# Kernel optimization log

Hardware: AMD Instinct MI355X
Metric: run time of the kernel (lower is better)

The kernel has to match this reference:

```python
import jax, jax.numpy as jnp
import numpy as np

N_NODES = 50000
N_EDGES = 500000
D = 128  # node/edge feature dim


def setup_inputs() -> dict:
    key = jax.random.key(0)
    k1, k2, k3, k4, k5 = jax.random.split(key, 5)
    x_node = jax.random.normal(k1, (N_NODES, D), dtype=jnp.float32)
    x_edge = jax.random.normal(k2, (N_EDGES, D), dtype=jnp.float32)
    edge_index = jax.random.randint(k3, (N_EDGES, 2), 0, N_NODES, dtype=jnp.int64)
    # MLP params: Linear(3D -> D) -> ReLU -> Linear(D -> D)
    W1 = jax.random.normal(k4, (3 * D, D), dtype=jnp.float32) * (1.0 / np.sqrt(3 * D))
    b1 = jnp.zeros((D,), dtype=jnp.float32)
    W2 = jax.random.normal(k5, (D, D), dtype=jnp.float32) * (1.0 / np.sqrt(D))
    b2 = jnp.zeros((D,), dtype=jnp.float32)
    return {"x_node": x_node, "x_edge": x_edge, "edge_index": edge_index,
            "W1": W1, "b1": b1, "W2": W2, "b2": b2}


def reference(x_node, x_edge, edge_index, W1, b1, W2, b2):
    # gather node features at both endpoints of each edge
    v0 = x_node[edge_index[:, 0]]          # [E, D]
    v1 = x_node[edge_index[:, 1]]          # [E, D]
    x_new = jnp.concatenate([v0, v1, x_edge], axis=1)  # [E, 3D]
    h = jax.nn.relu(x_new @ W1 + b1)       # [E, D]
    x_edge_new = h @ W2 + b2               # [E, D]
    return x_edge_new
```

## Files before the change

### kernel.cpp

```cpp
#include <hip/hip_runtime.h>
#include <stdint.h>

#define D 128
#define MT 64

typedef short short8 __attribute__((ext_vector_type(8)));
typedef float f32x16 __attribute__((ext_vector_type(16)));

__device__ __forceinline__ unsigned short f2bf(float f) {
    union { float f; uint32_t u; } v;
    v.f = f;
    uint32_t u = v.u;
    uint32_t r = (u + 0x7fffu + ((u >> 16) & 1u)) >> 16;
    return (unsigned short)r;
}

__global__ void pack_weights_kernel(const float* __restrict__ W1,
                                    const float* __restrict__ W2,
                                    unsigned short* __restrict__ W1p,
                                    unsigned short* __restrict__ W2p) {
    int t = blockIdx.x * 256 + threadIdx.x;
    if (t < 6144) {
        int kt = t >> 8, nt = (t >> 6) & 3, lane = t & 63;
        int n = nt * 32 + (lane & 31);
        int kb = kt * 16 + (lane >> 5) * 8;
        unsigned short* dst = W1p + t * 8;
        #pragma unroll
        for (int j = 0; j < 8; ++j) dst[j] = f2bf(W1[(kb + j) * D + n]);
    } else if (t < 8192) {
        int u = t - 6144;
        int kt = u >> 8, nt = (u >> 6) & 3, lane = u & 63;
        int n = nt * 32 + (lane & 31);
        int kb = kt * 16 + (lane >> 5) * 8;
        unsigned short* dst = W2p + u * 8;
        #pragma unroll
        for (int j = 0; j < 8; ++j) dst[j] = f2bf(W2[(kb + j) * D + n]);
    }
}

__global__ __launch_bounds__(512, 6) void edge_mlp_kernel(
    const float* __restrict__ x_node,
    const float* __restrict__ x_edge,
    const int* __restrict__ eidx,
    const unsigned short* __restrict__ W1p,
    const unsigned short* __restrict__ W2p,
    const float* __restrict__ b1,
    const float* __restrict__ b2,
    float* __restrict__ out,
    int E) {
    __shared__ unsigned short lds[MT * 392];
    unsigned short* Hs = lds;

    const int t = threadIdx.x;
    const int r0 = blockIdx.x * MT;

    const int w = t >> 6;
    const int cb = w & 3;
    const int rt = w >> 2;
    const int lane = t & 63;
    const int lrow = lane & 31;
    const int khalf = (lane >> 5) * 8;
    const int n = cb * 32 + lrow;
    const int rbump = (lane >> 5) * 4;
    const int arow = rt * 32 + lrow;

    const unsigned short* bp1 = W1p + ((size_t)cb * 64 + lane) * 8;
    const unsigned short* bp2 = W2p + ((size_t)cb * 64 + lane) * 8;

    short8 bbuf0 = *(const short8*)(bp1);
    short8 bbuf1 = *(const short8*)(bp1 + 1 * 2048);
    short8 bbuf2 = *(const short8*)(bp1 + 2 * 2048);
    short8 bbuf3 = *(const short8*)(bp1 + 3 * 2048);

    {
        const int lane32 = t & 31;
        const int rsub = t >> 5;

        int2 e[4];
        int rgc[4];
        #pragma unroll
        for (int rb = 0; rb < 4; ++rb) {
            int rg = r0 + rb * 16 + rsub;
            rgc[rb] = rg < E ? rg : E - 1;
            e[rb] = ((const int2*)eidx)[rgc[rb]];
        }
        float4 v0[4], v1[4], v2[4];
        #pragma unroll
        for (int rb = 0; rb < 4; ++rb) {
            v0[rb] = ((const float4*)(x_node + (size_t)e[rb].x * D))[lane32];
            v1[rb] = ((const float4*)(x_node + (size_t)e[rb].y * D))[lane32];
            v2[rb] = ((const float4*)(x_edge + (size_t)rgc[rb] * D))[lane32];
        }
        #pragma unroll
        for (int rb = 0; rb < 4; ++rb) {
            int row = rb * 16 + rsub;
            unsigned short* base = &lds[row * 392 + lane32 * 4];
            ushort4 p;
            p.x = f2bf(v0[rb].x); p.y = f2bf(v0[rb].y); p.z = f2bf(v0[rb].z); p.w = f2bf(v0[rb].w);
            *(ushort4*)(base) = p;
            p.x = f2bf(v1[rb].x); p.y = f2bf(v1[rb].y); p.z = f2bf(v1[rb].z); p.w = f2bf(v1[rb].w);
            *(ushort4*)(base + 128) = p;
            p.x = f2bf(v2[rb].x); p.y = f2bf(v2[rb].y); p.z = f2bf(v2[rb].z); p.w = f2bf(v2[rb].w);
            *(ushort4*)(base + 256) = p;
        }
    }
    __syncthreads();

    f32x16 acc;
    #pragma unroll
    for (int i = 0; i < 16; ++i) acc[i] = 0.f;

    #pragma unroll
    for (int kt = 0; kt < 24; ++kt) {
        short8 a = *(const short8*)&lds[arow * 392 + kt * 16 + khalf];
        short8 b;
        switch (kt & 3) {
            case 0: b = bbuf0; if (kt + 4 < 24) bbuf0 = *(const short8*)(bp1 + (kt + 4) * 2048); break;
            case 1: b = bbuf1; if (kt + 4 < 24) bbuf1 = *(const short8*)(bp1 + (kt + 4) * 2048); break;
            case 2: b = bbuf2; if (kt + 4 < 24) bbuf2 = *(const short8*)(bp1 + (kt + 4) * 2048); break;
            default: b = bbuf3; if (kt + 4 < 24) bbuf3 = *(const short8*)(bp1 + (kt + 4) * 2048); break;
        }
        acc = __builtin_amdgcn_mfma_f32_32x32x16_bf16(a, b, acc, 0, 0, 0);
    }

    short8 b2buf[8];
    #pragma unroll
    for (int i = 0; i < 8; ++i) b2buf[i] = *(const short8*)(bp2 + i * 2048);

    __syncthreads();

    {
        float b1v = b1[n];
        #pragma unroll
        for (int r = 0; r < 16; ++r) {
            int rr = rt * 32 + (r & 3) + 8 * (r >> 2) + rbump;
            Hs[rr * 136 + n] = f2bf(fmaxf(acc[r] + b1v, 0.f));
        }
    }
    __syncthreads();

    f32x16 c;
    #pragma unroll
    for (int i = 0; i < 16; ++i) c[i] = 0.f;

    #pragma unroll
    for (int kt = 0; kt < 8; ++kt) {
        short8 a = *(const short8*)&Hs[arow * 136 + kt * 16 + khalf];
        c = __builtin_amdgcn_mfma_f32_32x32x16_bf16(a, b2buf[kt], c, 0, 0, 0);
    }

    {
        float b2v = b2[n];
        #pragma unroll
        for (int r = 0; r < 16; ++r) {
            int rr = rt * 32 + (r & 3) + 8 * (r >> 2) + rbump;
            int rg = r0 + rr;
            if (rg < E) out[(size_t)rg * D + n] = c[r] + b2v;
        }
    }
}

extern "C" void kernel_launch(void* const* d_in, const int* in_sizes, int n_in,
                              void* d_out, int out_size, void* d_ws, size_t ws_size,
                              hipStream_t stream) {
    const float* x_node = (const float*)d_in[0];
    const float* x_edge = (const float*)d_in[1];
    const int*   eidx   = (const int*)d_in[2];
    const float* W1     = (const float*)d_in[3];
    const float* b1     = (const float*)d_in[4];
    const float* W2     = (const float*)d_in[5];
    const float* b2     = (const float*)d_in[6];
    float* out = (float*)d_out;

    const int E = in_sizes[1] / D;

    unsigned short* W1p = (unsigned short*)d_ws;
    unsigned short* W2p = W1p + 6144 * 8;

    pack_weights_kernel<<<32, 256, 0, stream>>>(W1, W2, W1p, W2p);

    int nblk = (E + MT - 1) / MT;
    edge_mlp_kernel<<<nblk, 512, 0, stream>>>(x_node, x_edge, eidx, W1p, W2p, b1, b2, out, E);
}
```

Before: 533.4 us.

## Make edge MLP kernel persistent with register-prefetched gathers for upcoming tiles

Launches a fixed grid of at most 512 blocks that loop over 64-edge tiles. Each iteration gathers the node and edge features for the next tile into registers, and the edge indices for the tile after that, while the current tile's two MFMA GEMMs run. X and H get separate LDS buffers so staging and compute do not alias. This aims to hide the latency of the random gathers behind compute. In exchange it lowers the launch-bound occupancy hint and reloads weight fragments from global memory on every tile instead of keeping them in a register ring.

```diff
diff --git a/kernel.cpp b/kernel.cpp
--- a/kernel.cpp
+++ b/kernel.cpp
@@ -3,6 +3,8 @@
 
 #define D 128
 #define MT 64
+#define XS 392
+#define HS 136
 
 typedef short short8 __attribute__((ext_vector_type(8)));
 typedef float f32x16 __attribute__((ext_vector_type(16)));
@@ -38,7 +40,7 @@
     }
 }
 
-__global__ __launch_bounds__(512, 6) void edge_mlp_kernel(
+__global__ __launch_bounds__(512, 4) void edge_mlp_kernel(
     const float* __restrict__ x_node,
     const float* __restrict__ x_edge,
     const int* __restrict__ eidx,
@@ -47,13 +49,16 @@
     const float* __restrict__ b1,
     const float* __restrict__ b2,
     float* __restrict__ out,
-    int E) {
-    __shared__ unsigned short lds[MT * 392];
-    unsigned short* Hs = lds;
+    int E, int nblk) {
+    __shared__ unsigned short Xs[MT * XS];
+    __shared__ unsigned short Hs[MT * HS];
 
     const int t = threadIdx.x;
-    const int r0 = blockIdx.x * MT;
+    const int g = gridDim.x;
+    const int bid = blockIdx.x;
 
+    const int lane32 = t & 31;
+    const int rsub = t >> 5;
     const int w = t >> 6;
     const int cb = w & 3;
     const int rt = w >> 2;
@@ -66,96 +71,104 @@
 
     const unsigned short* bp1 = W1p + ((size_t)cb * 64 + lane) * 8;
     const unsigned short* bp2 = W2p + ((size_t)cb * 64 + lane) * 8;
+    const float b1v = b1[n];
+    const float b2v = b2[n];
 
-    short8 bbuf0 = *(const short8*)(bp1);
-    short8 bbuf1 = *(const short8*)(bp1 + 1 * 2048);
-    short8 bbuf2 = *(const short8*)(bp1 + 2 * 2048);
-    short8 bbuf3 = *(const short8*)(bp1 + 3 * 2048);
+    int2 e[4];
+    int rg[4];
+    float4 v0[4], v1[4], v2[4];
 
     {
-        const int lane32 = t & 31;
-        const int rsub = t >> 5;
-
-        int2 e[4];
-        int rgc[4];
+        int tb = bid * MT;
         #pragma unroll
         for (int rb = 0; rb < 4; ++rb) {
-            int rg = r0 + rb * 16 + rsub;
-            rgc[rb] = rg < E ? rg : E - 1;
-            e[rb] = ((const int2*)eidx)[rgc[rb]];
+            int r = tb + rb * 16 + rsub;
+            rg[rb] = r < E ? r : E - 1;
+            e[rb] = ((const int2*)eidx)[rg[rb]];
         }
-        float4 v0[4], v1[4], v2[4];
         #pragma unroll
         for (int rb = 0; rb < 4; ++rb) {
             v0[rb] = ((const float4*)(x_node + (size_t)e[rb].x * D))[lane32];
             v1[rb] = ((const float4*)(x_node + (size_t)e[rb].y * D))[lane32];
-            v2[rb] = ((const float4*)(x_edge + (size_t)rgc[rb] * D))[lane32];
+            v2[rb] = ((const float4*)(x_edge + (size_t)rg[rb] * D))[lane32];
         }
+        int nt2 = bid + g < nblk ? bid + g : nblk - 1;
+        int tb2 = nt2 * MT;
         #pragma unroll
         for (int rb = 0; rb < 4; ++rb) {
-            int row = rb * 16 + rsub;
-            unsigned short* base = &lds[row * 392 + lane32 * 4];
+            int r = tb2 + rb * 16 + rsub;
+            rg[rb] = r < E ? r : E - 1;
+            e[rb] = ((const int2*)eidx)[rg[rb]];
+        }
+    }
+
+    for (int tile = bid; tile < nblk; tile += g) {
+        #pragma unroll
+        for (int rb = 0; rb < 4; ++rb) {
+            unsigned short* base = &Xs[(rb * 16 + rsub) * XS + lane32 * 4];
             ushort4 p;
-            p.x = f2bf(v0[rb].x); p.y = f2bf(v0[rb].y); p.z = f2bf(v0[rb].z); p.w = f2bf(v0[rb].w);
+            p.x = f2bf(v0[rb].x); p.y = f2bf(v0[rb].y);
+            p.z = f2bf(v0[rb].z); p.w = f2bf(v0[rb].w);
             *(ushort4*)(base) = p;
-            p.x = f2bf(v1[rb].x); p.y = f2bf(v1[rb].y); p.z = f2bf(v1[rb].z); p.w = f2bf(v1[rb].w);
+            p.x = f2bf(v1[rb].x); p.y = f2bf(v1[rb].y);
+            p.z = f2bf(v1[rb].z); p.w = f2bf(v1[rb].w);
             *(ushort4*)(base + 128) = p;
-            p.x = f2bf(v2[rb].x); p.y = f2bf(v2[rb].y); p.z = f2bf(v2[rb].z); p.w = f2bf(v2[rb].w);
+            p.x = f2bf(v2[rb].x); p.y = f2bf(v2[rb].y);
+            p.z = f2bf(v2[rb].z); p.w = f2bf(v2[rb].w);
             *(ushort4*)(base + 256) = p;
         }
-    }
-    __syncthreads();
+        __syncthreads();
 
-    f32x16 acc;
-    #pragma unroll
-    for (int i = 0; i < 16; ++i) acc[i] = 0.f;
+        #pragma unroll
+        for (int rb = 0; rb < 4; ++rb) {
+            v0[rb] = ((const float4*)(x_node + (size_t)e[rb].x * D))[lane32];
+            v1[rb] = ((const float4*)(x_node + (size_t)e[rb].y * D))[lane32];
+            v2[rb] = ((const float4*)(x_edge + (size_t)rg[rb] * D))[lane32];
+        }
+        {
+            int nt2 = tile + 2 * g < nblk ? tile + 2 * g : nblk - 1;
+            int tb2 = nt2 * MT;
+            #pragma unroll
+            for (int rb = 0; rb < 4; ++rb) {
+                int r = tb2 + rb * 16 + rsub;
+                rg[rb] = r < E ? r : E - 1;
+                e[rb] = ((const int2*)eidx)[rg[rb]];
+            }
+        }
 
-    #pragma unroll
-    for (int kt = 0; kt < 24; ++kt) {
-        short8 a = *(const short8*)&lds[arow * 392 + kt * 16 + khalf];
-        short8 b;
-        switch (kt & 3) {
-            case 0: b = bbuf0; if (kt + 4 < 24) bbuf0 = *(const short8*)(bp1 + (kt + 4) * 2048); break;
-            case 1: b = bbuf1; if (kt + 4 < 24) bbuf1 = *(const short8*)(bp1 + (kt + 4) * 2048); break;
-            case 2: b = bbuf2; if (kt + 4 < 24) bbuf2 = *(const short8*)(bp1 + (kt + 4) * 2048); break;
-            default: b = bbuf3; if (kt + 4 < 24) bbuf3 = *(const short8*)(bp1 + (kt + 4) * 2048); break;
+        f32x16 acc;
+        #pragma unroll
+        for (int i = 0; i < 16; ++i) acc[i] = 0.f;
+        #pragma unroll 8
+        for (int kt = 0; kt < 24; ++kt) {
+            short8 a = *(const short8*)&Xs[arow * XS + kt * 16 + khalf];
+            short8 b = *(const short8*)(bp1 + (size_t)kt * 2048);
+            acc = __builtin_amdgcn_mfma_f32_32x32x16_bf16(a, b, acc, 0, 0, 0);
         }
-        acc = __builtin_amdgcn_mfma_f32_32x32x16_bf16(a, b, acc, 0, 0, 0);
-    }
-
-    short8 b2buf[8];
-    #pragma unroll
-    for (int i = 0; i < 8; ++i) b2buf[i] = *(const short8*)(bp2 + i * 2048);
-
-    __syncthreads();
-
-    {
-        float b1v = b1[n];
         #pragma unroll
         for (int r = 0; r < 16; ++r) {
             int rr = rt * 32 + (r & 3) + 8 * (r >> 2) + rbump;
-            Hs[rr * 136 + n] = f2bf(fmaxf(acc[r] + b1v, 0.f));
+            Hs[rr * HS + n] = f2bf(fmaxf(acc[r] + b1v, 0.f));
         }
-    }
-    __syncthreads();
+        __syncthreads();
 
-    f32x16 c;
-    #pragma unroll
-    for (int i = 0; i < 16; ++i) c[i] = 0.f;
-
-    #pragma unroll
-    for (int kt = 0; kt < 8; ++kt) {
-        short8 a = *(const short8*)&Hs[arow * 136 + kt * 16 + khalf];
-        c = __builtin_amdgcn_mfma_f32_32x32x16_bf16(a, b2buf[kt], c, 0, 0, 0);
-    }
-
-    {
-        float b2v = b2[n];
+        f32x16 c;
         #pragma unroll
-        for (int r = 0; r < 16; ++r) {
-            int rr = rt * 32 + (r & 3) + 8 * (r >> 2) + rbump;
-            int rg = r0 + rr;
-            if (rg < E) out[(size_t)rg * D + n] = c[r] + b2v;
+        for (int i = 0; i < 16; ++i) c[i] = 0.f;
+        #pragma unroll
+        for (int kt = 0; kt < 8; ++kt) {
+            short8 a = *(const short8*)&Hs[arow * HS + kt * 16 + khalf];
+            short8 wb = *(const short8*)(bp2 + (size_t)kt * 2048);
+            c = __builtin_amdgcn_mfma_f32_32x32x16_bf16(a, wb, c, 0, 0, 0);
+        }
+        {
+            const int r0 = tile * MT;
+            #pragma unroll
+            for (int r = 0; r < 16; ++r) {
+                int rr = rt * 32 + (r & 3) + 8 * (r >> 2) + rbump;
+                int rgl = r0 + rr;
+                if (rgl < E) out[(size_t)rgl * D + n] = c[r] + b2v;
+            }
         }
     }
 }
@@ -180,5 +193,7 @@
     pack_weights_kernel<<<32, 256, 0, stream>>>(W1, W2, W1p, W2p);
 
     int nblk = (E + MT - 1) / MT;
-    edge_mlp_kernel<<<nblk, 512, 0, stream>>>(x_node, x_edge, eidx, W1p, W2p, b1, b2, out, E);
+    int grid = nblk < 512 ? nblk : 512;
+    if (grid < 1) grid = 1;
+    edge_mlp_kernel<<<grid, 512, 0, stream>>>(x_node, x_edge, eidx, W1p, W2p, b1, b2, out, E, nblk);
 }
```

Result: slower. 582.7 us (+9.2%).

## Halve edge tile to 32 rows with 256-thread blocks and inline weight loads

Applied to the files above, without the earlier changes.

Shrinks the per-block edge tile from 64 to 32 rows and the block from 512 to 256 threads, so each wave covers one 32-column slice of all 32 rows. The explicit register prefetch of W1/W2 fragments is dropped in favour of direct global loads inside a partially unrolled MFMA loop. The x_edge load is also moved ahead of the index load. The aim is less LDS per block, more resident blocks and finer grain for overlapping gather latency. In exchange, each block reloads the full weight set for half as many rows, doubling weight traffic per edge, and the MFMA loop loses its software prefetch.

```diff
diff --git a/kernel.cpp b/kernel.cpp
--- a/kernel.cpp
+++ b/kernel.cpp
@@ -2,7 +2,9 @@
 #include <stdint.h>
 
 #define D 128
-#define MT 64
+#define MT 32
+#define XS 392
+#define HS 136
 
 typedef short short8 __attribute__((ext_vector_type(8)));
 typedef float f32x16 __attribute__((ext_vector_type(16)));
@@ -38,7 +40,7 @@
     }
 }
 
-__global__ __launch_bounds__(512, 6) void edge_mlp_kernel(
+__global__ __launch_bounds__(256, 6) void edge_mlp_kernel(
     const float* __restrict__ x_node,
     const float* __restrict__ x_edge,
     const int* __restrict__ eidx,
@@ -48,93 +50,77 @@
     const float* __restrict__ b2,
     float* __restrict__ out,
     int E) {
-    __shared__ unsigned short lds[MT * 392];
+    __shared__ unsigned short lds[MT * XS];
     unsigned short* Hs = lds;
 
     const int t = threadIdx.x;
     const int r0 = blockIdx.x * MT;
 
-    const int w = t >> 6;
-    const int cb = w & 3;
-    const int rt = w >> 2;
-    const int lane = t & 63;
-    const int lrow = lane & 31;
-    const int khalf = (lane >> 5) * 8;
-    const int n = cb * 32 + lrow;
-    const int rbump = (lane >> 5) * 4;
-    const int arow = rt * 32 + lrow;
-
-    const unsigned short* bp1 = W1p + ((size_t)cb * 64 + lane) * 8;
-    const unsigned short* bp2 = W2p + ((size_t)cb * 64 + lane) * 8;
-
-    short8 bbuf0 = *(const short8*)(bp1);
-    short8 bbuf1 = *(const short8*)(bp1 + 1 * 2048);
-    short8 bbuf2 = *(const short8*)(bp1 + 2 * 2048);
-    short8 bbuf3 = *(const short8*)(bp1 + 3 * 2048);
-
     {
         const int lane32 = t & 31;
         const int rsub = t >> 5;
 
-        int2 e[4];
         int rgc[4];
+        float4 v2[4];
         #pragma unroll
         for (int rb = 0; rb < 4; ++rb) {
-            int rg = r0 + rb * 16 + rsub;
+            int rg = r0 + rb * 8 + rsub;
             rgc[rb] = rg < E ? rg : E - 1;
+            v2[rb] = ((const float4*)(x_edge + (size_t)rgc[rb] * D))[lane32];
+        }
+        int2 e[4];
+        #pragma unroll
+        for (int rb = 0; rb < 4; ++rb)
             e[rb] = ((const int2*)eidx)[rgc[rb]];
-        }
-        float4 v0[4], v1[4], v2[4];
+        float4 v0[4], v1[4];
         #pragma unroll
         for (int rb = 0; rb < 4; ++rb) {
             v0[rb] = ((const float4*)(x_node + (size_t)e[rb].x * D))[lane32];
             v1[rb] = ((const float4*)(x_node + (size_t)e[rb].y * D))[lane32];
-            v2[rb] = ((const float4*)(x_edge + (size_t)rgc[rb] * D))[lane32];
         }
         #pragma unroll
         for (int rb = 0; rb < 4; ++rb) {
-            int row = rb * 16 + rsub;
-            unsigned short* base = &lds[row * 392 + lane32 * 4];
+            int row = rb * 8 + rsub;
+            unsigned short* base = &lds[row * XS + lane32 * 4];
             ushort4 p;
-            p.x = f2bf(v0[rb].x); p.y = f2bf(v0[rb].y); p.z = f2bf(v0[rb].z); p.w = f2bf(v0[rb].w);
+            p.x = f2bf(v0[rb].x); p.y = f2bf(v0[rb].y);
+            p.z = f2bf(v0[rb].z); p.w = f2bf(v0[rb].w);
             *(ushort4*)(base) = p;
-            p.x = f2bf(v1[rb].x); p.y = f2bf(v1[rb].y); p.z = f2bf(v1[rb].z); p.w = f2bf(v1[rb].w);
+            p.x = f2bf(v1[rb].x); p.y = f2bf(v1[rb].y);
+            p.z = f2bf(v1[rb].z); p.w = f2bf(v1[rb].w);
             *(ushort4*)(base + 128) = p;
-            p.x = f2bf(v2[rb].x); p.y = f2bf(v2[rb].y); p.z = f2bf(v2[rb].z); p.w = f2bf(v2[rb].w);
+            p.x = f2bf(v2[rb].x); p.y = f2bf(v2[rb].y);
+            p.z = f2bf(v2[rb].z); p.w = f2bf(v2[rb].w);
             *(ushort4*)(base + 256) = p;
         }
     }
     __syncthreads();
 
+    const int w = t >> 6;
+    const int lane = t & 63;
+    const int lrow = lane & 31;
+    const int khalf = (lane >> 5) * 8;
+    const int n = w * 32 + lrow;
+    const int rbump = (lane >> 5) * 4;
+
     f32x16 acc;
     #pragma unroll
     for (int i = 0; i < 16; ++i) acc[i] = 0.f;
 
-    #pragma unroll
+    #pragma unroll 8
     for (int kt = 0; kt < 24; ++kt) {
-        short8 a = *(const short8*)&lds[arow * 392 + kt * 16 + khalf];
-        short8 b;
-        switch (kt & 3) {
-            case 0: b = bbuf0; if (kt + 4 < 24) bbuf0 = *(const short8*)(bp1 + (kt + 4) * 2048); break;
-            case 1: b = bbuf1; if (kt + 4 < 24) bbuf1 = *(const short8*)(bp1 + (kt + 4) * 2048); break;
-            case 2: b = bbuf2; if (kt + 4 < 24) bbuf2 = *(const short8*)(bp1 + (kt + 4) * 2048); break;
-            default: b = bbuf3; if (kt + 4 < 24) bbuf3 = *(const short8*)(bp1 + (kt + 4) * 2048); break;
-        }
+        short8 a = *(const short8*)&lds[lrow * XS + kt * 16 + khalf];
+        short8 b = *(const short8*)(W1p + ((kt * 4 + w) * 64 + lane) * 8);
         acc = __builtin_amdgcn_mfma_f32_32x32x16_bf16(a, b, acc, 0, 0, 0);
     }
-
-    short8 b2buf[8];
-    #pragma unroll
-    for (int i = 0; i < 8; ++i) b2buf[i] = *(const short8*)(bp2 + i * 2048);
-
     __syncthreads();
 
     {
         float b1v = b1[n];
         #pragma unroll
         for (int r = 0; r < 16; ++r) {
-            int rr = rt * 32 + (r & 3) + 8 * (r >> 2) + rbump;
-            Hs[rr * 136 + n] = f2bf(fmaxf(acc[r] + b1v, 0.f));
+            int rr = (r & 3) + 8 * (r >> 2) + rbump;
+            Hs[rr * HS + n] = f2bf(fmaxf(acc[r] + b1v, 0.f));
         }
     }
     __syncthreads();
@@ -145,15 +131,16 @@
 
     #pragma unroll
     for (int kt = 0; kt < 8; ++kt) {
-        short8 a = *(const short8*)&Hs[arow * 136 + kt * 16 + khalf];
-        c = __builtin_amdgcn_mfma_f32_32x32x16_bf16(a, b2buf[kt], c, 0, 0, 0);
+        short8 a = *(const short8*)&Hs[lrow * HS + kt * 16 + khalf];
+        short8 b = *(const short8*)(W2p + ((kt * 4 + w) * 64 + lane) * 8);
+        c = __builtin_amdgcn_mfma_f32_32x32x16_bf16(a, b, c, 0, 0, 0);
     }
 
     {
         float b2v = b2[n];
         #pragma unroll
         for (int r = 0; r < 16; ++r) {
-            int rr = rt * 32 + (r & 3) + 8 * (r >> 2) + rbump;
+            int rr = (r & 3) + 8 * (r >> 2) + rbump;
             int rg = r0 + rr;
             if (rg < E) out[(size_t)rg * D + n] = c[r] + b2v;
         }
@@ -180,5 +167,5 @@
     pack_weights_kernel<<<32, 256, 0, stream>>>(W1, W2, W1p, W2p);
 
     int nblk = (E + MT - 1) / MT;
-    edge_mlp_kernel<<<nblk, 512, 0, stream>>>(x_node, x_edge, eidx, W1p, W2p, b1, b2, out, E);
+    edge_mlp_kernel<<<nblk, 256, 0, stream>>>(x_node, x_edge, eidx, W1p, W2p, b1, b2, out, E);
 }
```

Measured after the change: 521.4 us. 1.02x faster.
